# Optimization experiments

Measured on AMD Instinct MI355X. Metric: run time of the kernel, lower is better.

The kernel has to match this reference:

```python
import jax, jax.numpy as jnp
import numpy as np

B, S, DM, H = 8, 1024, 256, 8
D = DM // H  # 32


def setup_inputs() -> dict:
    key = jax.random.key(0)
    ks = jax.random.split(key, 8)
    xav = (6.0 / (DM + DM)) ** 0.5  # xavier_uniform bound for square Linear
    return {
        "q": jax.random.normal(ks[0], (B, S, DM), jnp.float32),
        "k": jax.random.normal(ks[1], (B, S, DM), jnp.float32),
        "v": jax.random.normal(ks[2], (B, S, DM), jnp.float32),
        "mask": jnp.tril(jnp.ones((1, 1, S, S), jnp.int32)),  # causal: mask==0 is disallowed
        "zero_pad": 1,
        "k_index": 5,
        "Wk": jax.random.uniform(ks[3], (DM, DM), jnp.float32, -xav, xav),
        "bk": jnp.zeros((DM,), jnp.float32),
        "Wv": jax.random.uniform(ks[4], (DM, DM), jnp.float32, -xav, xav),
        "bv": jnp.zeros((DM,), jnp.float32),
        "Wo": jax.random.uniform(ks[5], (DM, DM), jnp.float32, -xav, xav),
        "bo": jnp.zeros((DM,), jnp.float32),
    }


def _attention4sparse_kt(qh, kh, vh, mask, zero_pad, k_index):
    # qh/kh/vh: [B,H,S,D]; mask: [1,1,S,S]
    d = qh.shape[-1]
    scores = jnp.einsum("bhid,bhjd->bhij", qh, kh) / jnp.sqrt(jnp.float32(d))
    scores = jnp.where(mask == 0, jnp.float32(-1e32), scores)
    attn = jax.nn.softmax(scores, axis=-1)  # [B,H,S,S]
    seqlen = attn.shape[2]
    if k_index + 1 < seqlen:
        # per-row k_index-th largest prob as threshold; keep top-k_index entries, re-softmax
        thresh = jax.lax.top_k(attn, k_index)[0][..., -1:]  # [B,H,S,1]
        sparse = jnp.where(attn - thresh >= 0.0, attn, jnp.float32(-1e16))
        resoft = jax.nn.softmax(sparse, axis=-1)
        rows = jnp.arange(seqlen)[None, None, :, None]
        # rows 0..k_index keep the original softmax; later rows use sparsified re-softmax
        attn = jnp.where(rows <= k_index, attn, resoft)
    if zero_pad:
        attn = attn.at[:, :, 0, :].set(0.0)
    out = jnp.einsum("bhij,bhjd->bhid", attn, vh)
    return out, attn


def reference(q, k, v, mask, zero_pad, k_index, Wk, bk, Wv, bv, Wo, bo):
    bs = q.shape[0]
    # key_query_same=True: q and k share k_linear
    kh = (k @ Wk.T + bk).reshape(bs, -1, H, D).transpose(0, 2, 1, 3)
    qh = (q @ Wk.T + bk).reshape(bs, -1, H, D).transpose(0, 2, 1, 3)
    vh = (v @ Wv.T + bv).reshape(bs, -1, H, D).transpose(0, 2, 1, 3)
    out, attn = _attention4sparse_kt(qh, kh, vh, mask, zero_pad, k_index)
    concat = out.transpose(0, 2, 1, 3).reshape(bs, -1, DM)
    output = concat @ Wo.T + bo
    return output, attn
```

## Files before the change

kernel.cpp:

```cpp
#include <hip/hip_runtime.h>
#include <cfloat>
#include <cmath>

#define S_LEN  1024
#define DHEAD  32
#define NHEAD  8
#define DMODEL 256
#define NBH    64
#define NROWS  8192

template<int HEADLAYOUT>
__global__ __launch_bounds__(256)
void gemm_xwT(const float* __restrict__ X, const float* __restrict__ W,
              const float* __restrict__ bias, float* __restrict__ C)
{
    __shared__ float Xs[32][68];
    __shared__ float Ws[32][68];
    const int tid  = threadIdx.x;
    const int tx   = tid & 15;
    const int ty   = tid >> 4;
    const int row0 = blockIdx.x * 64;
    const int col0 = blockIdx.y * 64;
    const int lr   = tid >> 2;
    const int seg  = tid & 3;

    float acc[4][4] = {{0.f,0.f,0.f,0.f},{0.f,0.f,0.f,0.f},
                       {0.f,0.f,0.f,0.f},{0.f,0.f,0.f,0.f}};

    for (int k0 = 0; k0 < DMODEL; k0 += 32) {
        const float4 x0 = *(const float4*)(X + (size_t)(row0 + lr) * DMODEL + k0 + seg * 8);
        const float4 x1 = *(const float4*)(X + (size_t)(row0 + lr) * DMODEL + k0 + seg * 8 + 4);
        const float4 w0 = *(const float4*)(W + (size_t)(col0 + lr) * DMODEL + k0 + seg * 8);
        const float4 w1 = *(const float4*)(W + (size_t)(col0 + lr) * DMODEL + k0 + seg * 8 + 4);
        __syncthreads();
        const int kk0 = seg * 8;
        Xs[kk0+0][lr]=x0.x; Xs[kk0+1][lr]=x0.y; Xs[kk0+2][lr]=x0.z; Xs[kk0+3][lr]=x0.w;
        Xs[kk0+4][lr]=x1.x; Xs[kk0+5][lr]=x1.y; Xs[kk0+6][lr]=x1.z; Xs[kk0+7][lr]=x1.w;
        Ws[kk0+0][lr]=w0.x; Ws[kk0+1][lr]=w0.y; Ws[kk0+2][lr]=w0.z; Ws[kk0+3][lr]=w0.w;
        Ws[kk0+4][lr]=w1.x; Ws[kk0+5][lr]=w1.y; Ws[kk0+6][lr]=w1.z; Ws[kk0+7][lr]=w1.w;
        __syncthreads();
        #pragma unroll
        for (int kk = 0; kk < 32; ++kk) {
            const float4 a = *(const float4*)&Xs[kk][ty*4];
            const float4 b = *(const float4*)&Ws[kk][tx*4];
            acc[0][0]+=a.x*b.x; acc[0][1]+=a.x*b.y; acc[0][2]+=a.x*b.z; acc[0][3]+=a.x*b.w;
            acc[1][0]+=a.y*b.x; acc[1][1]+=a.y*b.y; acc[1][2]+=a.y*b.z; acc[1][3]+=a.y*b.w;
            acc[2][0]+=a.z*b.x; acc[2][1]+=a.z*b.y; acc[2][2]+=a.z*b.z; acc[2][3]+=a.z*b.w;
            acc[3][0]+=a.w*b.x; acc[3][1]+=a.w*b.y; acc[3][2]+=a.w*b.z; acc[3][3]+=a.w*b.w;
        }
    }

    const float4 bv = *(const float4*)(bias + col0 + tx*4);
    #pragma unroll
    for (int iR = 0; iR < 4; ++iR) {
        const int r = row0 + ty*4 + iR;
        float4 o;
        o.x = acc[iR][0]+bv.x; o.y = acc[iR][1]+bv.y;
        o.z = acc[iR][2]+bv.z; o.w = acc[iR][3]+bv.w;
        if (HEADLAYOUT) {
            const int b = r >> 10, s = r & 1023;
            const int c = col0 + tx*4;
            const int h = c >> 5, d0 = c & 31;
            *(float4*)(C + (((size_t)(b*NHEAD + h))*S_LEN + s)*DHEAD + d0) = o;
        } else {
            *(float4*)(C + (size_t)r*DMODEL + col0 + tx*4) = o;
        }
    }
}

__global__ __launch_bounds__(512)
void attn_sparse_kernel(const float* __restrict__ qh, const float* __restrict__ kh,
                        const float* __restrict__ vh,
                        const int* __restrict__ zp_p, const int* __restrict__ ki_p,
                        float* __restrict__ attn, float* __restrict__ outp)
{
    __shared__ float smem[24704];
    float (*sc)[S_LEN] = (float (*)[S_LEN])smem;
    float (*kT)[260]   = (float (*)[260])(smem + 16*S_LEN);

    const int tid = threadIdx.x;
    const int qb  = blockIdx.x & 63;
    const int bh  = blockIdx.x >> 6;
    const int i0  = qb * 16;
    const int zp  = zp_p[0];
    int kidx = ki_p[0];
    if (kidx < 1) kidx = 1;
    if (kidx > 8) kidx = 8;

    const int cjs = tid & 63;
    const int rg  = tid >> 6;
    float qr0[DHEAD], qr1[DHEAD];
    {
        const float4* qp0 = (const float4*)(qh + (((size_t)bh)*S_LEN + i0 + rg*2 + 0)*DHEAD);
        const float4* qp1 = (const float4*)(qh + (((size_t)bh)*S_LEN + i0 + rg*2 + 1)*DHEAD);
        #pragma unroll
        for (int t4 = 0; t4 < 8; ++t4) {
            const float4 a = qp0[t4], b = qp1[t4];
            qr0[t4*4+0]=a.x; qr0[t4*4+1]=a.y; qr0[t4*4+2]=a.z; qr0[t4*4+3]=a.w;
            qr1[t4*4+0]=b.x; qr1[t4*4+1]=b.y; qr1[t4*4+2]=b.z; qr1[t4*4+3]=b.w;
        }
    }
    const int imax = i0 + 15;
    const int njt  = (imax >> 8) + 1;
    const int NJ   = njt << 8;
    const float SCALE = sqrtf((float)DHEAD);

    for (int t = 0; t < njt; ++t) {
        const int j0 = t << 8;
        {
            const int jj = tid >> 1;
            const int hf = tid & 1;
            const float4* kp = (const float4*)(kh + (((size_t)bh)*S_LEN + j0 + jj)*DHEAD + hf*16);
            #pragma unroll
            for (int q4 = 0; q4 < 4; ++q4) {
                const float4 v = kp[q4];
                const int kk = hf*16 + q4*4;
                kT[kk+0][jj]=v.x; kT[kk+1][jj]=v.y; kT[kk+2][jj]=v.z; kT[kk+3][jj]=v.w;
            }
        }
        __syncthreads();
        float s0[4]={0.f,0.f,0.f,0.f}, s1[4]={0.f,0.f,0.f,0.f};
        #pragma unroll
        for (int kk = 0; kk < DHEAD; ++kk) {
            const float4 kv = *(const float4*)&kT[kk][cjs*4];
            const float a0 = qr0[kk], a1 = qr1[kk];
            s0[0]+=a0*kv.x; s0[1]+=a0*kv.y; s0[2]+=a0*kv.z; s0[3]+=a0*kv.w;
            s1[0]+=a1*kv.x; s1[1]+=a1*kv.y; s1[2]+=a1*kv.z; s1[3]+=a1*kv.w;
        }
        {
            const int iA = i0 + rg*2;
            const int jb = j0 + cjs*4;
            #pragma unroll
            for (int e = 0; e < 4; ++e)
                sc[rg*2+0][jb+e] = (jb+e <= iA)   ? (s0[e]/SCALE) : -FLT_MAX;
            #pragma unroll
            for (int e = 0; e < 4; ++e)
                sc[rg*2+1][jb+e] = (jb+e <= iA+1) ? (s1[e]/SCALE) : -FLT_MAX;
        }
        __syncthreads();
    }

    const int r2 = tid >> 5;
    const int c2 = tid & 31;
    const int i  = i0 + r2;
    const int base = (r2 & 1) * 32;

    float m = -FLT_MAX;
    for (int j = c2; j < NJ; j += 32) m = fmaxf(m, sc[r2][j]);
    #pragma unroll
    for (int off = 16; off >= 1; off >>= 1) m = fmaxf(m, __shfl_xor(m, off, 32));

    float Z = 0.f;
    float tk[8];
    #pragma unroll
    for (int u = 0; u < 8; ++u) tk[u] = -FLT_MAX;
    for (int j = c2; j < NJ; j += 32) {
        const float v = sc[r2][j];
        Z += expf(v - m);
        if (v > tk[7]) {
            float w = v;
            #pragma unroll
            for (int u = 0; u < 8; ++u) {
                const float mx = fmaxf(tk[u], w);
                const float mn = fminf(tk[u], w);
                tk[u] = mx; w = mn;
            }
        }
    }
    #pragma unroll
    for (int off = 16; off >= 1; off >>= 1) Z += __shfl_xor(Z, off, 32);

    float thresh_s = -FLT_MAX;
    for (int round = 0; round < kidx; ++round) {
        float g = tk[0];
        #pragma unroll
        for (int off = 16; off >= 1; off >>= 1) g = fmaxf(g, __shfl_xor(g, off, 32));
        thresh_s = g;
        const bool match = (tk[0] == g);
        const unsigned long long bb = __ballot(match);
        const unsigned int m32 = (unsigned int)(bb >> base);
        const int leader = __ffs(m32) - 1;
        if (match && c2 == leader) {
            tk[0]=tk[1]; tk[1]=tk[2]; tk[2]=tk[3]; tk[3]=tk[4];
            tk[4]=tk[5]; tk[5]=tk[6]; tk[6]=tk[7]; tk[7]=-FLT_MAX;
        }
    }

    const float pmax     = 1.0f / Z;
    const float thresh_p = expf(thresh_s - m) / Z;
    const bool  sparse   = (i > kidx);

    float S2 = 0.f;
    if (sparse) {
        for (int j = c2; j <= i; j += 32) {
            const float p = expf(sc[r2][j] - m) / Z;
            if (p >= thresh_p) S2 += expf(p - pmax);
        }
        #pragma unroll
        for (int off = 16; off >= 1; off >>= 1) S2 += __shfl_xor(S2, off, 32);
    }

    float oa[DHEAD];
    #pragma unroll
    for (int d = 0; d < DHEAD; ++d) oa[d] = 0.f;

    const bool zero_row = (i == 0) && (zp != 0);
    for (int j = c2; j < NJ; j += 32) {
        float w = 0.f;
        if (!zero_row && j <= i) {
            const float p = expf(sc[r2][j] - m) / Z;
            if (!sparse)               w = p;
            else if (p >= thresh_p)    w = expf(p - pmax) / S2;
        }
        sc[r2][j] = w;
        if (w != 0.f) {
            const float4* vp = (const float4*)(vh + (((size_t)bh)*S_LEN + j)*DHEAD);
            #pragma unroll
            for (int t4 = 0; t4 < 8; ++t4) {
                const float4 v = vp[t4];
                oa[t4*4+0]+=w*v.x; oa[t4*4+1]+=w*v.y; oa[t4*4+2]+=w*v.z; oa[t4*4+3]+=w*v.w;
            }
        }
    }
    __syncthreads();

    {
        const float4 z4 = {0.f,0.f,0.f,0.f};
        for (int idx = tid; idx < 16*256; idx += 512) {
            const int r  = idx >> 8;
            const int f4 = idx & 255;
            float4 v = (f4*4 < NJ) ? *(const float4*)&sc[r][f4*4] : z4;
            *(float4*)(attn + (((size_t)bh)*S_LEN + i0 + r)*S_LEN + f4*4) = v;
        }
    }
    __syncthreads();

    float* red = smem;
    {
        const int rowoff = (r2*32 + c2)*33;
        #pragma unroll
        for (int d = 0; d < DHEAD; ++d) red[rowoff + d] = oa[d];
    }
    __syncthreads();
    {
        const int r3 = tid >> 5;
        const int d  = tid & 31;
        float sum = 0.f;
        #pragma unroll
        for (int c = 0; c < 32; ++c) sum += red[(r3*32 + c)*33 + d];
        const int b = bh >> 3, h = bh & 7;
        const int s = i0 + r3;
        outp[(((size_t)b)*S_LEN + s)*DMODEL + h*DHEAD + d] = sum;
    }
}

extern "C" void kernel_launch(void* const* d_in, const int* in_sizes, int n_in,
                              void* d_out, int out_size, void* d_ws, size_t ws_size,
                              hipStream_t stream)
{
    (void)in_sizes; (void)n_in; (void)out_size; (void)ws_size;

    const float* q  = (const float*)d_in[0];
    const float* k  = (const float*)d_in[1];
    const float* v  = (const float*)d_in[2];
    const int*   zp = (const int*)d_in[4];
    const int*   ki = (const int*)d_in[5];
    const float* Wk = (const float*)d_in[6];
    const float* bk = (const float*)d_in[7];
    const float* Wv = (const float*)d_in[8];
    const float* bv = (const float*)d_in[9];
    const float* Wo = (const float*)d_in[10];
    const float* bo = (const float*)d_in[11];

    float* out  = (float*)d_out;
    float* attn = (float*)d_out + 2097152;

    float* ws   = (float*)d_ws;
    float* qh   = ws;
    float* kh   = ws + 2097152;
    float* vhp  = ws + 2*2097152;
    float* outp = ws + 3*2097152;

    const dim3 gg(NROWS/64, DMODEL/64);
    hipLaunchKernelGGL((gemm_xwT<1>), gg, dim3(256), 0, stream, q, Wk, bk, qh);
    hipLaunchKernelGGL((gemm_xwT<1>), gg, dim3(256), 0, stream, k, Wk, bk, kh);
    hipLaunchKernelGGL((gemm_xwT<1>), gg, dim3(256), 0, stream, v, Wv, bv, vhp);

    hipLaunchKernelGGL(attn_sparse_kernel, dim3(NBH*64), dim3(512), 0, stream,
                       qh, kh, vhp, zp, ki, attn, outp);

    hipLaunchKernelGGL((gemm_xwT<0>), gg, dim3(256), 0, stream, outp, Wo, bo, out);
}
```

Measured before the change: 785.4 us.

## Rewrite projections as batched 128-tile GEMM and register-resident sparse attention

Merges the three input projections into one launch with 128x128 tiles and swizzled shared memory. The output projection gets a 128x64 tile. The attention kernel keeps each row's scores in registers across a 64-lane wavefront instead of a 64KB shared score buffer, which frees shared memory for occupancy. It computes softmax, top-k and the re-softmax from those registers and gathers only the nonzero V entries through ballot and shuffle. It also remaps block indices over batch-heads and writes attn rows directly. The costs are higher register pressure from 8x8 accumulators and a serialized per-nonzero gather loop, which is long for the unsparsified early rows.

Measured after the change: 724.9 us. 1.08x faster.

```diff
diff --git a/kernel.cpp b/kernel.cpp
--- a/kernel.cpp
+++ b/kernel.cpp
@@ -6,252 +6,357 @@
 #define DHEAD  32
 #define NHEAD  8
 #define DMODEL 256
-#define NBH    64
-#define NROWS  8192
-
-template<int HEADLAYOUT>
+
 __global__ __launch_bounds__(256)
-void gemm_xwT(const float* __restrict__ X, const float* __restrict__ W,
+void proj_gemm(const float* __restrict__ q, const float* __restrict__ k, const float* __restrict__ v,
+               const float* __restrict__ Wk, const float* __restrict__ bk,
+               const float* __restrict__ Wv, const float* __restrict__ bv,
+               float* __restrict__ qh, float* __restrict__ kh, float* __restrict__ vh)
+{
+    __shared__ float Xs[128*36];
+    __shared__ float Ws_[128*36];
+    const int z = blockIdx.z;
+    const float* X    = (z==0) ? q  : ((z==1) ? k  : v);
+    const float* W    = (z==2) ? Wv : Wk;
+    const float* bias = (z==2) ? bv : bk;
+    float*       C    = (z==0) ? qh : ((z==1) ? kh : vh);
+
+    const int tid  = threadIdx.x;
+    const int row0 = blockIdx.x * 128;
+    const int col0 = blockIdx.y * 128;
+    const int tx = tid & 15, ty = tid >> 4;
+    const int sr = tid >> 1, shf = tid & 1;
+
+    float acc[8][8];
+    #pragma unroll
+    for (int a = 0; a < 8; ++a)
+        #pragma unroll
+        for (int b = 0; b < 8; ++b) acc[a][b] = 0.f;
+
+    const int xg = ty & 7;
+    const int wg = tx & 7;
+    const int swb = (sr >> 3) & 7;
+
+    for (int k0 = 0; k0 < DMODEL; k0 += 32) {
+        const float4* xp = (const float4*)(X + (size_t)(row0 + sr) * DMODEL + k0 + shf*16);
+        const float4* wp = (const float4*)(W + (size_t)(col0 + sr) * DMODEL + k0 + shf*16);
+        float4 xv[4], wv[4];
+        #pragma unroll
+        for (int q4 = 0; q4 < 4; ++q4) { xv[q4] = xp[q4]; wv[q4] = wp[q4]; }
+        if (k0) __syncthreads();
+        #pragma unroll
+        for (int q4 = 0; q4 < 4; ++q4) {
+            const int slot = (shf*4 + q4) ^ swb;
+            *(float4*)&Xs [sr*36 + slot*4] = xv[q4];
+            *(float4*)&Ws_[sr*36 + slot*4] = wv[q4];
+        }
+        __syncthreads();
+        #pragma unroll
+        for (int g = 0; g < 8; ++g) {
+            float4 xf[8];
+            #pragma unroll
+            for (int ri = 0; ri < 8; ++ri)
+                xf[ri] = *(const float4*)&Xs[(ty*8+ri)*36 + ((g ^ xg) << 2)];
+            #pragma unroll
+            for (int ci = 0; ci < 8; ++ci) {
+                const float4 wf = *(const float4*)&Ws_[(tx*8+ci)*36 + ((g ^ wg) << 2)];
+                #pragma unroll
+                for (int ri = 0; ri < 8; ++ri) {
+                    acc[ri][ci] += xf[ri].x * wf.x;
+                    acc[ri][ci] += xf[ri].y * wf.y;
+                    acc[ri][ci] += xf[ri].z * wf.z;
+                    acc[ri][ci] += xf[ri].w * wf.w;
+                }
+            }
+        }
+    }
+
+    #pragma unroll
+    for (int ri = 0; ri < 8; ++ri) {
+        const int r = row0 + ty*8 + ri;
+        const int bI = r >> 10, s = r & 1023;
+        #pragma unroll
+        for (int half = 0; half < 2; ++half) {
+            const int c = col0 + tx*8 + half*4;
+            const float4 bv4 = *(const float4*)(bias + c);
+            float4 o;
+            o.x = acc[ri][half*4+0] + bv4.x;
+            o.y = acc[ri][half*4+1] + bv4.y;
+            o.z = acc[ri][half*4+2] + bv4.z;
+            o.w = acc[ri][half*4+3] + bv4.w;
+            const int h = c >> 5, d0 = c & 31;
+            *(float4*)(C + (((size_t)(bI*NHEAD + h))*S_LEN + s)*DHEAD + d0) = o;
+        }
+    }
+}
+
+__global__ __launch_bounds__(256)
+void out_gemm(const float* __restrict__ X, const float* __restrict__ W,
               const float* __restrict__ bias, float* __restrict__ C)
 {
-    __shared__ float Xs[32][68];
-    __shared__ float Ws[32][68];
+    __shared__ float Xs[128*36];
+    __shared__ float Ws_[64*36];
     const int tid  = threadIdx.x;
-    const int tx   = tid & 15;
-    const int ty   = tid >> 4;
-    const int row0 = blockIdx.x * 64;
+    const int row0 = blockIdx.x * 128;
     const int col0 = blockIdx.y * 64;
-    const int lr   = tid >> 2;
-    const int seg  = tid & 3;
-
-    float acc[4][4] = {{0.f,0.f,0.f,0.f},{0.f,0.f,0.f,0.f},
-                       {0.f,0.f,0.f,0.f},{0.f,0.f,0.f,0.f}};
+    const int tx = tid & 15, ty = tid >> 4;
+    const int sr = tid >> 1, shf = tid & 1;
+    const int wc = tid >> 2, wq = tid & 3;
+
+    float acc[8][4];
+    #pragma unroll
+    for (int a = 0; a < 8; ++a)
+        #pragma unroll
+        for (int b = 0; b < 4; ++b) acc[a][b] = 0.f;
+
+    const int xg  = ty & 7;
+    const int wg2 = (tx >> 1) & 7;
+    const int swbx = (sr >> 3) & 7;
+    const int swbw = (wc >> 3) & 7;
 
     for (int k0 = 0; k0 < DMODEL; k0 += 32) {
-        const float4 x0 = *(const float4*)(X + (size_t)(row0 + lr) * DMODEL + k0 + seg * 8);
-        const float4 x1 = *(const float4*)(X + (size_t)(row0 + lr) * DMODEL + k0 + seg * 8 + 4);
-        const float4 w0 = *(const float4*)(W + (size_t)(col0 + lr) * DMODEL + k0 + seg * 8);
-        const float4 w1 = *(const float4*)(W + (size_t)(col0 + lr) * DMODEL + k0 + seg * 8 + 4);
+        const float4* xp = (const float4*)(X + (size_t)(row0 + sr) * DMODEL + k0 + shf*16);
+        const float4* wp = (const float4*)(W + (size_t)(col0 + wc) * DMODEL + k0 + wq*8);
+        float4 xv[4], wv[2];
+        #pragma unroll
+        for (int q4 = 0; q4 < 4; ++q4) xv[q4] = xp[q4];
+        #pragma unroll
+        for (int q2 = 0; q2 < 2; ++q2) wv[q2] = wp[q2];
+        if (k0) __syncthreads();
+        #pragma unroll
+        for (int q4 = 0; q4 < 4; ++q4) {
+            const int slot = (shf*4 + q4) ^ swbx;
+            *(float4*)&Xs[sr*36 + slot*4] = xv[q4];
+        }
+        #pragma unroll
+        for (int q2 = 0; q2 < 2; ++q2) {
+            const int slot = (wq*2 + q2) ^ swbw;
+            *(float4*)&Ws_[wc*36 + slot*4] = wv[q2];
+        }
         __syncthreads();
-        const int kk0 = seg * 8;
-        Xs[kk0+0][lr]=x0.x; Xs[kk0+1][lr]=x0.y; Xs[kk0+2][lr]=x0.z; Xs[kk0+3][lr]=x0.w;
-        Xs[kk0+4][lr]=x1.x; Xs[kk0+5][lr]=x1.y; Xs[kk0+6][lr]=x1.z; Xs[kk0+7][lr]=x1.w;
-        Ws[kk0+0][lr]=w0.x; Ws[kk0+1][lr]=w0.y; Ws[kk0+2][lr]=w0.z; Ws[kk0+3][lr]=w0.w;
-        Ws[kk0+4][lr]=w1.x; Ws[kk0+5][lr]=w1.y; Ws[kk0+6][lr]=w1.z; Ws[kk0+7][lr]=w1.w;
-        __syncthreads();
-        #pragma unroll
-        for (int kk = 0; kk < 32; ++kk) {
-            const float4 a = *(const float4*)&Xs[kk][ty*4];
-            const float4 b = *(const float4*)&Ws[kk][tx*4];
-            acc[0][0]+=a.x*b.x; acc[0][1]+=a.x*b.y; acc[0][2]+=a.x*b.z; acc[0][3]+=a.x*b.w;
-            acc[1][0]+=a.y*b.x; acc[1][1]+=a.y*b.y; acc[1][2]+=a.y*b.z; acc[1][3]+=a.y*b.w;
-            acc[2][0]+=a.z*b.x; acc[2][1]+=a.z*b.y; acc[2][2]+=a.z*b.z; acc[2][3]+=a.z*b.w;
-            acc[3][0]+=a.w*b.x; acc[3][1]+=a.w*b.y; acc[3][2]+=a.w*b.z; acc[3][3]+=a.w*b.w;
-        }
-    }
-
-    const float4 bv = *(const float4*)(bias + col0 + tx*4);
-    #pragma unroll
-    for (int iR = 0; iR < 4; ++iR) {
-        const int r = row0 + ty*4 + iR;
+        #pragma unroll
+        for (int g = 0; g < 8; ++g) {
+            float4 xf[8];
+            #pragma unroll
+            for (int ri = 0; ri < 8; ++ri)
+                xf[ri] = *(const float4*)&Xs[(ty*8+ri)*36 + ((g ^ xg) << 2)];
+            #pragma unroll
+            for (int ci = 0; ci < 4; ++ci) {
+                const float4 wf = *(const float4*)&Ws_[(tx*4+ci)*36 + ((g ^ wg2) << 2)];
+                #pragma unroll
+                for (int ri = 0; ri < 8; ++ri) {
+                    acc[ri][ci] += xf[ri].x * wf.x;
+                    acc[ri][ci] += xf[ri].y * wf.y;
+                    acc[ri][ci] += xf[ri].z * wf.z;
+                    acc[ri][ci] += xf[ri].w * wf.w;
+                }
+            }
+        }
+    }
+
+    #pragma unroll
+    for (int ri = 0; ri < 8; ++ri) {
+        const int r = row0 + ty*8 + ri;
+        const int c = col0 + tx*4;
+        const float4 bv4 = *(const float4*)(bias + c);
         float4 o;
-        o.x = acc[iR][0]+bv.x; o.y = acc[iR][1]+bv.y;
-        o.z = acc[iR][2]+bv.z; o.w = acc[iR][3]+bv.w;
-        if (HEADLAYOUT) {
-            const int b = r >> 10, s = r & 1023;
-            const int c = col0 + tx*4;
-            const int h = c >> 5, d0 = c & 31;
-            *(float4*)(C + (((size_t)(b*NHEAD + h))*S_LEN + s)*DHEAD + d0) = o;
-        } else {
-            *(float4*)(C + (size_t)r*DMODEL + col0 + tx*4) = o;
-        }
-    }
+        o.x = acc[ri][0] + bv4.x; o.y = acc[ri][1] + bv4.y;
+        o.z = acc[ri][2] + bv4.z; o.w = acc[ri][3] + bv4.w;
+        *(float4*)(C + (size_t)r * DMODEL + c) = o;
+    }
+}
+
+__device__ __forceinline__ float process_row(
+    float (&s)[4][4], const int i, const int l, const int kidx, const int zp,
+    const float* __restrict__ vbase, float* __restrict__ arow)
+{
+    const int vcol = l & 31;
+    float m = -FLT_MAX;
+    #pragma unroll
+    for (int t = 0; t < 4; ++t)
+        #pragma unroll
+        for (int e = 0; e < 4; ++e) m = fmaxf(m, s[t][e]);
+    #pragma unroll
+    for (int off = 32; off >= 1; off >>= 1) m = fmaxf(m, __shfl_xor(m, off, 64));
+
+    float e_[4][4]; float Z = 0.f;
+    #pragma unroll
+    for (int t = 0; t < 4; ++t)
+        #pragma unroll
+        for (int e = 0; e < 4; ++e) { const float x = expf(s[t][e] - m); e_[t][e] = x; Z += x; }
+    #pragma unroll
+    for (int off = 32; off >= 1; off >>= 1) Z += __shfl_xor(Z, off, 64);
+
+    float p[4][4];
+    #pragma unroll
+    for (int t = 0; t < 4; ++t)
+        #pragma unroll
+        for (int e = 0; e < 4; ++e) p[t][e] = e_[t][e] / Z;
+
+    float tk[8];
+    #pragma unroll
+    for (int u = 0; u < 8; ++u) tk[u] = -FLT_MAX;
+    #pragma unroll
+    for (int t = 0; t < 4; ++t)
+        #pragma unroll
+        for (int e = 0; e < 4; ++e) {
+            const float v = p[t][e];
+            if (v > tk[7]) {
+                float w = v;
+                #pragma unroll
+                for (int u = 0; u < 8; ++u) {
+                    const float mx = fmaxf(tk[u], w);
+                    const float mn = fminf(tk[u], w);
+                    tk[u] = mx; w = mn;
+                }
+            }
+        }
+    float thresh = -FLT_MAX;
+    for (int round = 0; round < kidx; ++round) {
+        float g = tk[0];
+        #pragma unroll
+        for (int off = 32; off >= 1; off >>= 1) g = fmaxf(g, __shfl_xor(g, off, 64));
+        thresh = g;
+        const unsigned long long bb = __ballot(tk[0] == g);
+        const int leader = (int)__ffsll(bb) - 1;
+        if (l == leader) {
+            tk[0]=tk[1]; tk[1]=tk[2]; tk[2]=tk[3]; tk[3]=tk[4];
+            tk[4]=tk[5]; tk[5]=tk[6]; tk[6]=tk[7]; tk[7]=-FLT_MAX;
+        }
+    }
+
+    const bool  sparse = (i > kidx);
+    const float pmax   = 1.0f / Z;
+    float S2 = 0.f;
+    if (sparse) {
+        #pragma unroll
+        for (int t = 0; t < 4; ++t)
+            #pragma unroll
+            for (int e = 0; e < 4; ++e)
+                if (p[t][e] - thresh >= 0.f) S2 += expf(p[t][e] - pmax);
+        #pragma unroll
+        for (int off = 32; off >= 1; off >>= 1) S2 += __shfl_xor(S2, off, 64);
+    }
+
+    const bool zr = (i == 0) && (zp != 0);
+    float w[4][4];
+    #pragma unroll
+    for (int t = 0; t < 4; ++t)
+        #pragma unroll
+        for (int e = 0; e < 4; ++e) {
+            float ww;
+            if (zr)          ww = 0.f;
+            else if (!sparse) ww = p[t][e];
+            else              ww = (p[t][e] - thresh >= 0.f) ? expf(p[t][e] - pmax) / S2 : 0.f;
+            w[t][e] = ww;
+        }
+    #pragma unroll
+    for (int t = 0; t < 4; ++t) {
+        float4 f; f.x = w[t][0]; f.y = w[t][1]; f.z = w[t][2]; f.w = w[t][3];
+        *(float4*)(arow + t*256 + 4*l) = f;
+    }
+    float o = 0.f;
+    #pragma unroll
+    for (int t = 0; t < 4; ++t)
+        #pragma unroll
+        for (int e = 0; e < 4; ++e) {
+            unsigned long long mask = __ballot(w[t][e] != 0.f);
+            while (mask) {
+                const int src = (int)__ffsll(mask) - 1;
+                mask &= mask - 1;
+                const float wb = __shfl(w[t][e], src, 64);
+                const int j = t*256 + 4*src + e;
+                o += wb * vbase[(size_t)j * DHEAD + vcol];
+            }
+        }
+    return o;
 }
 
 __global__ __launch_bounds__(512)
-void attn_sparse_kernel(const float* __restrict__ qh, const float* __restrict__ kh,
-                        const float* __restrict__ vh,
-                        const int* __restrict__ zp_p, const int* __restrict__ ki_p,
-                        float* __restrict__ attn, float* __restrict__ outp)
-{
-    __shared__ float smem[24704];
-    float (*sc)[S_LEN] = (float (*)[S_LEN])smem;
-    float (*kT)[260]   = (float (*)[260])(smem + 16*S_LEN);
-
+void attn_sparse_v2(const float* __restrict__ qh, const float* __restrict__ kh,
+                    const float* __restrict__ vh,
+                    const int* __restrict__ zp_p, const int* __restrict__ ki_p,
+                    float* __restrict__ attn, float* __restrict__ outp)
+{
+    __shared__ float kT[32*264];
     const int tid = threadIdx.x;
-    const int qb  = blockIdx.x & 63;
-    const int bh  = blockIdx.x >> 6;
-    const int i0  = qb * 16;
-    const int zp  = zp_p[0];
+    const int l = tid & 63, w = tid >> 6;
+    const int g0 = blockIdx.x;
+    const int bh = ((g0 & 7) << 3) + ((g0 >> 3) & 7);
+    const int qb = g0 >> 6;
+    const int i0 = qb * 16;
+    const int iA = i0 + 2*w, iB = iA + 1;
+    const int zp = zp_p[0];
     int kidx = ki_p[0];
     if (kidx < 1) kidx = 1;
     if (kidx > 8) kidx = 8;
-
-    const int cjs = tid & 63;
-    const int rg  = tid >> 6;
-    float qr0[DHEAD], qr1[DHEAD];
+    const float SCALE = sqrtf((float)DHEAD);
+
+    const float* kb = kh + (size_t)bh * S_LEN * DHEAD;
+    const float* vb = vh + (size_t)bh * S_LEN * DHEAD;
+
+    float qa[32], qbr[32];
     {
-        const float4* qp0 = (const float4*)(qh + (((size_t)bh)*S_LEN + i0 + rg*2 + 0)*DHEAD);
-        const float4* qp1 = (const float4*)(qh + (((size_t)bh)*S_LEN + i0 + rg*2 + 1)*DHEAD);
+        const float4* qpA = (const float4*)(qh + ((size_t)bh*S_LEN + iA)*DHEAD);
+        const float4* qpB = (const float4*)(qh + ((size_t)bh*S_LEN + iB)*DHEAD);
         #pragma unroll
         for (int t4 = 0; t4 < 8; ++t4) {
-            const float4 a = qp0[t4], b = qp1[t4];
-            qr0[t4*4+0]=a.x; qr0[t4*4+1]=a.y; qr0[t4*4+2]=a.z; qr0[t4*4+3]=a.w;
-            qr1[t4*4+0]=b.x; qr1[t4*4+1]=b.y; qr1[t4*4+2]=b.z; qr1[t4*4+3]=b.w;
-        }
-    }
-    const int imax = i0 + 15;
-    const int njt  = (imax >> 8) + 1;
-    const int NJ   = njt << 8;
-    const float SCALE = sqrtf((float)DHEAD);
-
-    for (int t = 0; t < njt; ++t) {
-        const int j0 = t << 8;
-        {
-            const int jj = tid >> 1;
-            const int hf = tid & 1;
-            const float4* kp = (const float4*)(kh + (((size_t)bh)*S_LEN + j0 + jj)*DHEAD + hf*16);
-            #pragma unroll
-            for (int q4 = 0; q4 < 4; ++q4) {
-                const float4 v = kp[q4];
-                const int kk = hf*16 + q4*4;
-                kT[kk+0][jj]=v.x; kT[kk+1][jj]=v.y; kT[kk+2][jj]=v.z; kT[kk+3][jj]=v.w;
-            }
-        }
-        __syncthreads();
-        float s0[4]={0.f,0.f,0.f,0.f}, s1[4]={0.f,0.f,0.f,0.f};
-        #pragma unroll
-        for (int kk = 0; kk < DHEAD; ++kk) {
-            const float4 kv = *(const float4*)&kT[kk][cjs*4];
-            const float a0 = qr0[kk], a1 = qr1[kk];
-            s0[0]+=a0*kv.x; s0[1]+=a0*kv.y; s0[2]+=a0*kv.z; s0[3]+=a0*kv.w;
-            s1[0]+=a1*kv.x; s1[1]+=a1*kv.y; s1[2]+=a1*kv.z; s1[3]+=a1*kv.w;
-        }
-        {
-            const int iA = i0 + rg*2;
-            const int jb = j0 + cjs*4;
-            #pragma unroll
-            for (int e = 0; e < 4; ++e)
-                sc[rg*2+0][jb+e] = (jb+e <= iA)   ? (s0[e]/SCALE) : -FLT_MAX;
-            #pragma unroll
-            for (int e = 0; e < 4; ++e)
-                sc[rg*2+1][jb+e] = (jb+e <= iA+1) ? (s1[e]/SCALE) : -FLT_MAX;
-        }
-        __syncthreads();
-    }
-
-    const int r2 = tid >> 5;
-    const int c2 = tid & 31;
-    const int i  = i0 + r2;
-    const int base = (r2 & 1) * 32;
-
-    float m = -FLT_MAX;
-    for (int j = c2; j < NJ; j += 32) m = fmaxf(m, sc[r2][j]);
-    #pragma unroll
-    for (int off = 16; off >= 1; off >>= 1) m = fmaxf(m, __shfl_xor(m, off, 32));
-
-    float Z = 0.f;
-    float tk[8];
-    #pragma unroll
-    for (int u = 0; u < 8; ++u) tk[u] = -FLT_MAX;
-    for (int j = c2; j < NJ; j += 32) {
-        const float v = sc[r2][j];
-        Z += expf(v - m);
-        if (v > tk[7]) {
-            float w = v;
-            #pragma unroll
-            for (int u = 0; u < 8; ++u) {
-                const float mx = fmaxf(tk[u], w);
-                const float mn = fminf(tk[u], w);
-                tk[u] = mx; w = mn;
-            }
-        }
-    }
-    #pragma unroll
-    for (int off = 16; off >= 1; off >>= 1) Z += __shfl_xor(Z, off, 32);
-
-    float thresh_s = -FLT_MAX;
-    for (int round = 0; round < kidx; ++round) {
-        float g = tk[0];
-        #pragma unroll
-        for (int off = 16; off >= 1; off >>= 1) g = fmaxf(g, __shfl_xor(g, off, 32));
-        thresh_s = g;
-        const bool match = (tk[0] == g);
-        const unsigned long long bb = __ballot(match);
-        const unsigned int m32 = (unsigned int)(bb >> base);
-        const int leader = __ffs(m32) - 1;
-        if (match && c2 == leader) {
-            tk[0]=tk[1]; tk[1]=tk[2]; tk[2]=tk[3]; tk[3]=tk[4];
-            tk[4]=tk[5]; tk[5]=tk[6]; tk[6]=tk[7]; tk[7]=-FLT_MAX;
-        }
-    }
-
-    const float pmax     = 1.0f / Z;
-    const float thresh_p = expf(thresh_s - m) / Z;
-    const bool  sparse   = (i > kidx);
-
-    float S2 = 0.f;
-    if (sparse) {
-        for (int j = c2; j <= i; j += 32) {
-            const float p = expf(sc[r2][j] - m) / Z;
-            if (p >= thresh_p) S2 += expf(p - pmax);
-        }
-        #pragma unroll
-        for (int off = 16; off >= 1; off >>= 1) S2 += __shfl_xor(S2, off, 32);
-    }
-
-    float oa[DHEAD];
-    #pragma unroll
-    for (int d = 0; d < DHEAD; ++d) oa[d] = 0.f;
-
-    const bool zero_row = (i == 0) && (zp != 0);
-    for (int j = c2; j < NJ; j += 32) {
-        float w = 0.f;
-        if (!zero_row && j <= i) {
-            const float p = expf(sc[r2][j] - m) / Z;
-            if (!sparse)               w = p;
-            else if (p >= thresh_p)    w = expf(p - pmax) / S2;
-        }
-        sc[r2][j] = w;
-        if (w != 0.f) {
-            const float4* vp = (const float4*)(vh + (((size_t)bh)*S_LEN + j)*DHEAD);
-            #pragma unroll
-            for (int t4 = 0; t4 < 8; ++t4) {
-                const float4 v = vp[t4];
-                oa[t4*4+0]+=w*v.x; oa[t4*4+1]+=w*v.y; oa[t4*4+2]+=w*v.z; oa[t4*4+3]+=w*v.w;
-            }
-        }
-    }
-    __syncthreads();
-
-    {
-        const float4 z4 = {0.f,0.f,0.f,0.f};
-        for (int idx = tid; idx < 16*256; idx += 512) {
-            const int r  = idx >> 8;
-            const int f4 = idx & 255;
-            float4 v = (f4*4 < NJ) ? *(const float4*)&sc[r][f4*4] : z4;
-            *(float4*)(attn + (((size_t)bh)*S_LEN + i0 + r)*S_LEN + f4*4) = v;
-        }
-    }
-    __syncthreads();
-
-    float* red = smem;
-    {
-        const int rowoff = (r2*32 + c2)*33;
-        #pragma unroll
-        for (int d = 0; d < DHEAD; ++d) red[rowoff + d] = oa[d];
-    }
-    __syncthreads();
-    {
-        const int r3 = tid >> 5;
-        const int d  = tid & 31;
-        float sum = 0.f;
-        #pragma unroll
-        for (int c = 0; c < 32; ++c) sum += red[(r3*32 + c)*33 + d];
-        const int b = bh >> 3, h = bh & 7;
-        const int s = i0 + r3;
-        outp[(((size_t)b)*S_LEN + s)*DMODEL + h*DHEAD + d] = sum;
-    }
+            const float4 a = qpA[t4], b = qpB[t4];
+            qa [t4*4+0]=a.x; qa [t4*4+1]=a.y; qa [t4*4+2]=a.z; qa [t4*4+3]=a.w;
+            qbr[t4*4+0]=b.x; qbr[t4*4+1]=b.y; qbr[t4*4+2]=b.z; qbr[t4*4+3]=b.w;
+        }
+    }
+
+    float sA[4][4], sB[4][4];
+    #pragma unroll
+    for (int t = 0; t < 4; ++t)
+        #pragma unroll
+        for (int e = 0; e < 4; ++e) { sA[t][e] = -FLT_MAX; sB[t][e] = -FLT_MAX; }
+
+    #pragma unroll
+    for (int t = 0; t < 4; ++t) {
+        if (t*256 <= i0 + 15) {
+            if (t > 0) __syncthreads();
+            {
+                const int jj = tid >> 1, hf = tid & 1;
+                const float4* kp = (const float4*)(kb + ((size_t)(t*256 + jj))*DHEAD + hf*16);
+                const float4 k0 = kp[0], k1 = kp[1], k2 = kp[2], k3 = kp[3];
+                float* cb = &kT[jj];
+                const int rb = hf*16;
+                cb[(rb+ 0)*264]=k0.x; cb[(rb+ 1)*264]=k0.y; cb[(rb+ 2)*264]=k0.z; cb[(rb+ 3)*264]=k0.w;
+                cb[(rb+ 4)*264]=k1.x; cb[(rb+ 5)*264]=k1.y; cb[(rb+ 6)*264]=k1.z; cb[(rb+ 7)*264]=k1.w;
+                cb[(rb+ 8)*264]=k2.x; cb[(rb+ 9)*264]=k2.y; cb[(rb+10)*264]=k2.z; cb[(rb+11)*264]=k2.w;
+                cb[(rb+12)*264]=k3.x; cb[(rb+13)*264]=k3.y; cb[(rb+14)*264]=k3.z; cb[(rb+15)*264]=k3.w;
+            }
+            __syncthreads();
+            if (t*256 <= iB) {
+                float dA[4] = {0.f,0.f,0.f,0.f}, dB[4] = {0.f,0.f,0.f,0.f};
+                #pragma unroll
+                for (int kk = 0; kk < 32; ++kk) {
+                    const float4 kv = *(const float4*)&kT[kk*264 + 4*l];
+                    dA[0] += qa[kk]*kv.x; dA[1] += qa[kk]*kv.y;
+                    dA[2] += qa[kk]*kv.z; dA[3] += qa[kk]*kv.w;
+                    dB[0] += qbr[kk]*kv.x; dB[1] += qbr[kk]*kv.y;
+                    dB[2] += qbr[kk]*kv.z; dB[3] += qbr[kk]*kv.w;
+                }
+                #pragma unroll
+                for (int e = 0; e < 4; ++e) {
+                    const int j = t*256 + 4*l + e;
+                    if (j <= iA) sA[t][e] = dA[e] / SCALE;
+                    if (j <= iB) sB[t][e] = dB[e] / SCALE;
+                }
+            }
+        }
+    }
+
+    float* arowA = attn + ((size_t)bh*S_LEN + iA)*S_LEN;
+    float* arowB = attn + ((size_t)bh*S_LEN + iB)*S_LEN;
+    const float oA = process_row(sA, iA, l, kidx, zp, vb, arowA);
+    const float oB = process_row(sB, iB, l, kidx, zp, vb, arowB);
+
+    const int srow = iA + (l >> 5);
+    const float oval = (l < 32) ? oA : oB;
+    outp[((size_t)(bh >> 3)*S_LEN + srow)*DMODEL + (bh & 7)*DHEAD + (l & 31)] = oval;
 }
 
 extern "C" void kernel_launch(void* const* d_in, const int* in_sizes, int n_in,
@@ -281,13 +386,12 @@
     float* vhp  = ws + 2*2097152;
     float* outp = ws + 3*2097152;
 
-    const dim3 gg(NROWS/64, DMODEL/64);
-    hipLaunchKernelGGL((gemm_xwT<1>), gg, dim3(256), 0, stream, q, Wk, bk, qh);
-    hipLaunchKernelGGL((gemm_xwT<1>), gg, dim3(256), 0, stream, k, Wk, bk, kh);
-    hipLaunchKernelGGL((gemm_xwT<1>), gg, dim3(256), 0, stream, v, Wv, bv, vhp);
-
-    hipLaunchKernelGGL(attn_sparse_kernel, dim3(NBH*64), dim3(512), 0, stream,
+    hipLaunchKernelGGL(proj_gemm, dim3(64, 2, 3), dim3(256), 0, stream,
+                       q, k, v, Wk, bk, Wv, bv, qh, kh, vhp);
+
+    hipLaunchKernelGGL(attn_sparse_v2, dim3(4096), dim3(512), 0, stream,
                        qh, kh, vhp, zp, ki, attn, outp);
 
-    hipLaunchKernelGGL((gemm_xwT<0>), gg, dim3(256), 0, stream, outp, Wo, bo, out);
-}
+    hipLaunchKernelGGL(out_gemm, dim3(64, 4), dim3(256), 0, stream,
+                       outp, Wo, bo, out);
+}
```
